# Performance work log

Measured on AMD Instinct MI355X. Metric: run time of the kernel, lower is better.

## Reference

```python
import jax, jax.numpy as jnp
import numpy as np

VOCAB = 100000
TOPK = 20
EMB = 300
BS, SEQ = 64, 256

def setup_inputs() -> dict:
    key = jax.random.key(0)
    k1, k2, k3, k4, k5 = jax.random.split(key, 5)
    conceptnet_text_vec = jax.random.randint(k1, (BS, SEQ), 0, VOCAB)
    neighbors = jax.random.randint(k2, (VOCAB, TOPK), 0, VOCAB)
    emb = jax.random.normal(k3, (VOCAB, EMB), dtype=jnp.float32)
    # xavier-normal init for attention params
    a = jax.random.normal(k4, (EMB, EMB), dtype=jnp.float32) * np.sqrt(2.0 / (EMB + EMB))
    b = jax.random.normal(k5, (EMB, 1), dtype=jnp.float32) * np.sqrt(2.0 / (EMB + 1))
    return {"conceptnet_text_vec": conceptnet_text_vec, "neighbors": neighbors,
            "emb": emb, "a": a, "b": b}

def reference(conceptnet_text_vec, neighbors, emb, a, b):
    # double gather: ids -> neighbor ids -> neighbor embeddings
    nb = neighbors[conceptnet_text_vec]          # [B, S, K] int
    h = emb[nb]                                  # [B, S, K, D]
    # tanh attention scores over the K (neighbor) dim
    e = jnp.einsum('bske,e->bsk', jnp.tanh(jnp.einsum('bskd,de->bske', h, a)), b[:, 0])
    att = jax.nn.softmax(e, axis=-1)             # [B, S, K]
    return jnp.einsum('bsk,bskd->bsd', att, h)   # [B, S, D]
```

## Files before the change

kernel.cpp:

```cpp
#include <hip/hip_runtime.h>
#include <hip/hip_bf16.h>
#include <math.h>

#define VOCAB 100000
#define TOPK  20
#define EMB   300
#define NTOK  (64*256)
#define NB    1563
#define NSLICE 128

typedef __attribute__((ext_vector_type(8))) short short8;
typedef __attribute__((ext_vector_type(4))) short short4v;
typedef __attribute__((ext_vector_type(4))) float f32x4;

static __device__ inline short f2bf(float f) {
    __hip_bfloat16 h = __float2bfloat16(f);
    short s; __builtin_memcpy(&s, &h, 2);
    return s;
}

__global__ void prep_kernel(const float* __restrict__ A, short* __restrict__ aT)
{
    const int e = blockIdx.x;
    for (int d = threadIdx.x; d < 320; d += 256) {
        float f = (e < EMB && d < EMB) ? A[(size_t)d * EMB + e] : 0.f;
        aT[e * 320 + d] = f2bf(f);
    }
}

__global__ __launch_bounds__(512, 1) void score_kernel(
    const float* __restrict__ emb, const short* __restrict__ aT,
    const float* __restrict__ B, float* __restrict__ S0, float* __restrict__ S1)
{
    __shared__ short8 EsS[64 * 40];
    __shared__ float4 Scr[2 * 5 * 4 * 64];
    __shared__ float  Sred[128];

    const int t     = threadIdx.x;
    const int eh    = blockIdx.x >> 7;
    const int slice = blockIdx.x & 127;

    const int lid = t & 63;
    const int w   = t >> 6;
    const int kh  = w >> 2;
    const int mg  = (w >> 1) & 1;
    const int ng  = w & 1;
    const int lm  = lid & 15;
    const int lk  = lid >> 4;
    const int kb    = kh * 20;
    const int xmask = lm & 7;
    const int cell  = mg * 2 + ng;

    const short8* aT8 = (const short8*)aT;
    short8 bAll[5][5];
#pragma unroll
    for (int g = 0; g < 5; ++g) {
        const int e = eh * 160 + ng * 80 + g * 16 + lm;
#pragma unroll
        for (int ks = 0; ks < 5; ++ks)
            bAll[g][ks] = aT8[e * 40 + kb + ks * 4 + lk];
    }

    float bcol[5];
#pragma unroll
    for (int g = 0; g < 5; ++g) {
        const int e = eh * 160 + ng * 80 + g * 16 + lm;
        bcol[g] = (e < EMB) ? B[e] : 0.f;
    }
    int rb[2];
#pragma unroll
    for (int mt = 0; mt < 2; ++mt)
        rb[mt] = (mg * 32 + mt * 16 + lm) * 40;

    const int ntiles = (NB - slice + NSLICE - 1) / NSLICE;

    float4 pf[5][2]; float4 pft;

#define ISSUE_PF(tn) do {                                                     \
    const float4* esrc = (const float4*)(emb + (size_t)(tn) * 64 * EMB);      \
    _Pragma("unroll")                                                         \
    for (int j = 0; j < 5; ++j) {                                             \
        const int i = t + j * 512;                                            \
        const int row = i / 37, cc = i - row * 37;                            \
        const bool ok = (i < 2368) && ((tn) * 64 + row < VOCAB);              \
        pf[j][0] = ok ? esrc[row * 75 + cc * 2]     : make_float4(0,0,0,0);   \
        pf[j][1] = ok ? esrc[row * 75 + cc * 2 + 1] : make_float4(0,0,0,0);   \
    }                                                                         \
    if (t < 64) pft = ((tn) * 64 + t < VOCAB) ? esrc[t * 75 + 74]             \
                                              : make_float4(0,0,0,0);         \
} while (0)

#define STAGE() do {                                                          \
    _Pragma("unroll")                                                         \
    for (int j = 0; j < 5; ++j) {                                             \
        const int i = t + j * 512;                                            \
        if (i < 2368) {                                                       \
            const int row = i / 37, cc = i - row * 37;                        \
            short8 val;                                                       \
            val[0]=f2bf(pf[j][0].x); val[1]=f2bf(pf[j][0].y);                 \
            val[2]=f2bf(pf[j][0].z); val[3]=f2bf(pf[j][0].w);                 \
            val[4]=f2bf(pf[j][1].x); val[5]=f2bf(pf[j][1].y);                 \
            val[6]=f2bf(pf[j][1].z); val[7]=f2bf(pf[j][1].w);                 \
            EsS[row * 40 + (cc ^ (row & 7))] = val;                           \
        }                                                                     \
    }                                                                         \
    if (t < 64) {                                                             \
        short4v h; h.x=f2bf(pft.x); h.y=f2bf(pft.y);                          \
        h.z=f2bf(pft.z); h.w=f2bf(pft.w);                                     \
        short* base = (short*)&EsS[t * 40 + (37 ^ (t & 7))];                  \
        *(short4v*)(base) = h;                                                \
        *(short4v*)(base + 4) = (short4v){0,0,0,0};                           \
    }                                                                         \
    if (t < 128) {                                                            \
        const int row = t >> 1, cc = 38 + (t & 1);                            \
        EsS[row * 40 + (cc ^ (row & 7))] = (short8){0,0,0,0,0,0,0,0};         \
    }                                                                         \
} while (0)

    ISSUE_PF(slice);
    STAGE();
    ISSUE_PF(slice + NSLICE);
    __syncthreads();

    for (int tt = 0; tt < ntiles; ++tt) {
        const int tile = slice + tt * NSLICE;
        const int v0   = tile * 64;

        f32x4 acc0[5], acc1[5];
#pragma unroll
        for (int g = 0; g < 5; ++g) {
            acc0[g] = (f32x4){0.f, 0.f, 0.f, 0.f};
            acc1[g] = (f32x4){0.f, 0.f, 0.f, 0.f};
        }
        short8 afr[2][2];
        {
            const int kx = (kb + lk) ^ xmask;
            afr[0][0] = EsS[rb[0] + kx];
            afr[0][1] = EsS[rb[1] + kx];
        }
#pragma unroll
        for (int ks = 0; ks < 5; ++ks) {
            const int cur = ks & 1, nx = cur ^ 1;
            if (ks < 4) {
                const int kx = (kb + (ks + 1) * 4 + lk) ^ xmask;
                afr[nx][0] = EsS[rb[0] + kx];
                afr[nx][1] = EsS[rb[1] + kx];
            }
#pragma unroll
            for (int g = 0; g < 5; ++g) {
                acc0[g] = __builtin_amdgcn_mfma_f32_16x16x32_bf16(
                              afr[cur][0], bAll[g][ks], acc0[g], 0, 0, 0);
                acc1[g] = __builtin_amdgcn_mfma_f32_16x16x32_bf16(
                              afr[cur][1], bAll[g][ks], acc1[g], 0, 0, 0);
            }
        }
        __syncthreads();

        if (kh == 0) {
#pragma unroll
            for (int g = 0; g < 5; ++g)
                Scr[((0 * 5 + g) * 4 + cell) * 64 + lid] = *(float4*)&acc1[g];
        } else {
#pragma unroll
            for (int g = 0; g < 5; ++g)
                Scr[((1 * 5 + g) * 4 + cell) * 64 + lid] = *(float4*)&acc0[g];
        }
        if (tt + 1 < ntiles) {
            STAGE();
            ISSUE_PF(slice + (tt + 2) * NSLICE);
        }
        __syncthreads();

        float part[4];
        if (kh == 0) {
#pragma unroll
            for (int i = 0; i < 4; ++i) {
                float p = 0.f;
#pragma unroll
                for (int g = 0; g < 5; ++g) {
                    float4 o = Scr[((1 * 5 + g) * 4 + cell) * 64 + lid];
                    float x  = acc0[g][i] + ((const float*)&o)[i];
                    float xc = fminf(fmaxf(x, -15.f), 15.f);
                    float e2 = __expf(2.f * xc);
                    p += __fdividef(e2 - 1.f, e2 + 1.f) * bcol[g];
                }
                part[i] = p;
            }
        } else {
#pragma unroll
            for (int i = 0; i < 4; ++i) {
                float p = 0.f;
#pragma unroll
                for (int g = 0; g < 5; ++g) {
                    float4 o = Scr[((0 * 5 + g) * 4 + cell) * 64 + lid];
                    float x  = acc1[g][i] + ((const float*)&o)[i];
                    float xc = fminf(fmaxf(x, -15.f), 15.f);
                    float e2 = __expf(2.f * xc);
                    p += __fdividef(e2 - 1.f, e2 + 1.f) * bcol[g];
                }
                part[i] = p;
            }
        }
#pragma unroll
        for (int m = 1; m <= 8; m <<= 1)
#pragma unroll
            for (int i = 0; i < 4; ++i)
                part[i] += __shfl_xor(part[i], m);
        if (lm == 0) {
#pragma unroll
            for (int i = 0; i < 4; ++i)
                Sred[ng * 64 + mg * 32 + kh * 16 + lk * 4 + i] = part[i];
        }
        __syncthreads();

        if (t < 64) {
            const int v = v0 + t;
            if (v < VOCAB) {
                float* Sp = eh ? S1 : S0;
                Sp[v] = Sred[t] + Sred[64 + t];
            }
        }
    }
#undef ISSUE_PF
#undef STAGE
}

__global__ __launch_bounds__(256) void attend_kernel(
    const int* __restrict__ text, const int* __restrict__ neighbors,
    const float* __restrict__ emb, const float* __restrict__ S0,
    const float* __restrict__ S1, float* __restrict__ out)
{
    const int lane = threadIdx.x & 63;
    const int wv   = threadIdx.x >> 6;
    const int tok  = blockIdx.x * 4 + wv;

    const int tid = text[tok];

    int   nbk = 0;
    float sc  = -1e30f;
    if (lane < TOPK) {
        nbk = neighbors[tid * TOPK + lane];
        sc  = S0[nbk] + S1[nbk];
    }

    float mx = sc;
#pragma unroll
    for (int m = 16; m >= 1; m >>= 1)
        mx = fmaxf(mx, __shfl_xor(mx, m));

    float ex = (lane < TOPK) ? expf(sc - mx) : 0.f;
    float sum = ex;
#pragma unroll
    for (int m = 16; m >= 1; m >>= 1)
        sum += __shfl_xor(sum, m);
    float att = ex / sum;

    float acc0 = 0.f, acc1 = 0.f, acc2 = 0.f, acc3 = 0.f, acc4 = 0.f;
    const bool has5 = (lane < EMB - 256);
#pragma unroll 4
    for (int k = 0; k < TOPK; ++k) {
        const float wgt = __shfl(att, k);
        const int   id  = __shfl(nbk, k);
        const float* row = emb + (size_t)id * EMB;
        acc0 = fmaf(wgt, row[lane      ], acc0);
        acc1 = fmaf(wgt, row[lane +  64], acc1);
        acc2 = fmaf(wgt, row[lane + 128], acc2);
        acc3 = fmaf(wgt, row[lane + 192], acc3);
        if (has5) acc4 = fmaf(wgt, row[lane + 256], acc4);
    }

    float* orow = out + (size_t)tok * EMB;
    orow[lane      ] = acc0;
    orow[lane +  64] = acc1;
    orow[lane + 128] = acc2;
    orow[lane + 192] = acc3;
    if (has5) orow[lane + 256] = acc4;
}

extern "C" void kernel_launch(void* const* d_in, const int* in_sizes, int n_in,
                              void* d_out, int out_size, void* d_ws, size_t ws_size,
                              hipStream_t stream) {
    const int*   text      = (const int*)d_in[0];
    const int*   neighbors = (const int*)d_in[1];
    const float* emb       = (const float*)d_in[2];
    const float* A         = (const float*)d_in[3];
    const float* B         = (const float*)d_in[4];
    float*       out       = (float*)d_out;

    char* ws = (char*)d_ws;
    float* S0 = (float*)ws;
    float* S1 = (float*)(ws + 400000);
    short* aT = (short*)(ws + 800000);

    prep_kernel<<<320, 256, 0, stream>>>(A, aT);
    score_kernel<<<256, 512, 0, stream>>>(emb, aT, B, S0, S1);
    attend_kernel<<<NTOK / 4, 256, 0, stream>>>(text, neighbors, emb, S0, S1, out);
}
```

Baseline: 142.9 us.

## Restructure score kernel: 1024-thread blocks, B matrix in LDS, more blocks

The score kernel now launches 512 blocks of 1024 threads instead of 256 blocks of 512. Each block stages its half of the transposed A matrix into shared memory, and B fragments are read from LDS per k-step instead of being held in 25 registers per thread. Each wave now covers a single 16-row M tile, and the cross-k-half reduction scratch reuses the embedding tile buffer. The prefetch depth drops from two tiles ahead to one. The aim is to cut register pressure and raise parallelism, at the cost of more LDS traffic, an extra barrier per tile and less latency hiding on the emb loads.

```diff
diff --git a/kernel.cpp b/kernel.cpp
--- a/kernel.cpp
+++ b/kernel.cpp
@@ -7,7 +7,7 @@
 #define EMB   300
 #define NTOK  (64*256)
 #define NB    1563
-#define NSLICE 128
+#define NVG   256
 
 typedef __attribute__((ext_vector_type(8))) short short8;
 typedef __attribute__((ext_vector_type(4))) short short4v;
@@ -28,188 +28,155 @@
     }
 }
 
-__global__ __launch_bounds__(512, 1) void score_kernel(
+__global__ __launch_bounds__(1024, 1) void score_kernel(
     const float* __restrict__ emb, const short* __restrict__ aT,
     const float* __restrict__ B, float* __restrict__ S0, float* __restrict__ S1)
 {
+    __shared__ short8 BsS[160 * 40];
     __shared__ short8 EsS[64 * 40];
-    __shared__ float4 Scr[2 * 5 * 4 * 64];
     __shared__ float  Sred[128];
 
-    const int t     = threadIdx.x;
-    const int eh    = blockIdx.x >> 7;
-    const int slice = blockIdx.x & 127;
+    const int t  = threadIdx.x;
+    const int eh = blockIdx.x & 1;
+    const int vg = blockIdx.x >> 1;
+
+    const short8* aT8 = (const short8*)aT;
+#pragma unroll
+    for (int j = 0; j < 7; ++j) {
+        const int i = t + j * 1024;
+        if (i < 6400) {
+            const int col = i / 40, q = i - col * 40;
+            BsS[col * 40 + (q ^ (col & 7))] = aT8[(eh * 160 + col) * 40 + q];
+        }
+    }
 
     const int lid = t & 63;
     const int w   = t >> 6;
-    const int kh  = w >> 2;
-    const int mg  = (w >> 1) & 1;
+    const int kh  = w >> 3;
+    const int mg  = (w >> 1) & 3;
     const int ng  = w & 1;
     const int lm  = lid & 15;
     const int lk  = lid >> 4;
-    const int kb    = kh * 20;
-    const int xmask = lm & 7;
-    const int cell  = mg * 2 + ng;
-
-    const short8* aT8 = (const short8*)aT;
-    short8 bAll[5][5];
+    const int kb  = kh * 20;
+    const int xm  = lm & 7;
+    const int cell = mg * 2 + ng;
+
+    const int rbA = (mg * 16 + lm) * 40;
+    int rbB[5]; float bcol[5];
 #pragma unroll
     for (int g = 0; g < 5; ++g) {
-        const int e = eh * 160 + ng * 80 + g * 16 + lm;
-#pragma unroll
-        for (int ks = 0; ks < 5; ++ks)
-            bAll[g][ks] = aT8[e * 40 + kb + ks * 4 + lk];
-    }
-
-    float bcol[5];
-#pragma unroll
-    for (int g = 0; g < 5; ++g) {
-        const int e = eh * 160 + ng * 80 + g * 16 + lm;
+        const int col = ng * 80 + g * 16 + lm;
+        rbB[g] = col * 40;
+        const int e = eh * 160 + col;
         bcol[g] = (e < EMB) ? B[e] : 0.f;
     }
-    int rb[2];
-#pragma unroll
-    for (int mt = 0; mt < 2; ++mt)
-        rb[mt] = (mg * 32 + mt * 16 + lm) * 40;
-
-    const int ntiles = (NB - slice + NSLICE - 1) / NSLICE;
-
-    float4 pf[5][2]; float4 pft;
-
-#define ISSUE_PF(tn) do {                                                     \
-    const float4* esrc = (const float4*)(emb + (size_t)(tn) * 64 * EMB);      \
+
+    const int ntiles = (NB - vg + NVG - 1) / NVG;
+
+    float4 pf[3][2]; float4 pft;
+
+#define ISSUE_PF(TT) do {                                                     \
+    const float4* esrc = (const float4*)(emb + (size_t)(TT) * 64 * EMB);      \
     _Pragma("unroll")                                                         \
-    for (int j = 0; j < 5; ++j) {                                             \
-        const int i = t + j * 512;                                            \
-        const int row = i / 37, cc = i - row * 37;                            \
-        const bool ok = (i < 2368) && ((tn) * 64 + row < VOCAB);              \
-        pf[j][0] = ok ? esrc[row * 75 + cc * 2]     : make_float4(0,0,0,0);   \
-        pf[j][1] = ok ? esrc[row * 75 + cc * 2 + 1] : make_float4(0,0,0,0);   \
-    }                                                                         \
-    if (t < 64) pft = ((tn) * 64 + t < VOCAB) ? esrc[t * 75 + 74]             \
+    for (int j = 0; j < 3; ++j) {                                             \
+        const int i = t + j * 1024;                                           \
+        const int row = i / 37, c = i - row * 37;                             \
+        const bool ok = (i < 2368) && ((TT) * 64 + row < VOCAB);              \
+        pf[j][0] = ok ? esrc[row * 75 + c * 2]     : make_float4(0,0,0,0);    \
+        pf[j][1] = ok ? esrc[row * 75 + c * 2 + 1] : make_float4(0,0,0,0);    \
+    }                                                                         \
+    if (t < 64) pft = ((TT) * 64 + t < VOCAB) ? esrc[t * 75 + 74]             \
                                               : make_float4(0,0,0,0);         \
 } while (0)
 
 #define STAGE() do {                                                          \
     _Pragma("unroll")                                                         \
-    for (int j = 0; j < 5; ++j) {                                             \
-        const int i = t + j * 512;                                            \
+    for (int j = 0; j < 3; ++j) {                                             \
+        const int i = t + j * 1024;                                           \
         if (i < 2368) {                                                       \
-            const int row = i / 37, cc = i - row * 37;                        \
+            const int row = i / 37, c = i - row * 37;                         \
             short8 val;                                                       \
             val[0]=f2bf(pf[j][0].x); val[1]=f2bf(pf[j][0].y);                 \
             val[2]=f2bf(pf[j][0].z); val[3]=f2bf(pf[j][0].w);                 \
             val[4]=f2bf(pf[j][1].x); val[5]=f2bf(pf[j][1].y);                 \
             val[6]=f2bf(pf[j][1].z); val[7]=f2bf(pf[j][1].w);                 \
-            EsS[row * 40 + (cc ^ (row & 7))] = val;                           \
+            EsS[row * 40 + (c ^ (row & 7))] = val;                            \
         }                                                                     \
     }                                                                         \
-    if (t < 64) {                                                             \
-        short4v h; h.x=f2bf(pft.x); h.y=f2bf(pft.y);                          \
-        h.z=f2bf(pft.z); h.w=f2bf(pft.w);                                     \
-        short* base = (short*)&EsS[t * 40 + (37 ^ (t & 7))];                  \
-        *(short4v*)(base) = h;                                                \
-        *(short4v*)(base + 4) = (short4v){0,0,0,0};                           \
-    }                                                                         \
-    if (t < 128) {                                                            \
-        const int row = t >> 1, cc = 38 + (t & 1);                            \
-        EsS[row * 40 + (cc ^ (row & 7))] = (short8){0,0,0,0,0,0,0,0};         \
+    if (t < 64) {                   \
+        short8 v37 = (short8){0,0,0,0,0,0,0,0};                               \
+        v37[0]=f2bf(pft.x); v37[1]=f2bf(pft.y);                               \
+        v37[2]=f2bf(pft.z); v37[3]=f2bf(pft.w);                               \
+        EsS[t * 40 + (37 ^ (t & 7))] = v37;                                   \
+    }                                                                         \
+    if (t < 128) {                           \
+        const int row = t >> 1, q = 38 + (t & 1);                             \
+        EsS[row * 40 + (q ^ (row & 7))] = (short8){0,0,0,0,0,0,0,0};          \
     }                                                                         \
 } while (0)
 
-    ISSUE_PF(slice);
+    ISSUE_PF(vg);
     STAGE();
-    ISSUE_PF(slice + NSLICE);
-    __syncthreads();
 
     for (int tt = 0; tt < ntiles; ++tt) {
-        const int tile = slice + tt * NSLICE;
-        const int v0   = tile * 64;
-
-        f32x4 acc0[5], acc1[5];
-#pragma unroll
-        for (int g = 0; g < 5; ++g) {
-            acc0[g] = (f32x4){0.f, 0.f, 0.f, 0.f};
-            acc1[g] = (f32x4){0.f, 0.f, 0.f, 0.f};
-        }
-        short8 afr[2][2];
-        {
-            const int kx = (kb + lk) ^ xmask;
-            afr[0][0] = EsS[rb[0] + kx];
-            afr[0][1] = EsS[rb[1] + kx];
-        }
+        const int v0 = (vg + tt * NVG) * 64;
+
+        __syncthreads();
+        if (tt + 1 < ntiles) ISSUE_PF(vg + (tt + 1) * NVG);
+
+        f32x4 acc[5];
+#pragma unroll
+        for (int g = 0; g < 5; ++g) acc[g] = (f32x4){0.f, 0.f, 0.f, 0.f};
+
+        short8 afr[2];
+        afr[0] = EsS[rbA + ((kb + lk) ^ xm)];
 #pragma unroll
         for (int ks = 0; ks < 5; ++ks) {
             const int cur = ks & 1, nx = cur ^ 1;
-            if (ks < 4) {
-                const int kx = (kb + (ks + 1) * 4 + lk) ^ xmask;
-                afr[nx][0] = EsS[rb[0] + kx];
-                afr[nx][1] = EsS[rb[1] + kx];
-            }
+            if (ks < 4)
+                afr[nx] = EsS[rbA + ((kb + (ks + 1) * 4 + lk) ^ xm)];
+            short8 bfr[5];
+            const int sx = (kb + ks * 4 + lk) ^ xm;
+#pragma unroll
+            for (int g = 0; g < 5; ++g) bfr[g] = BsS[rbB[g] + sx];
+#pragma unroll
+            for (int g = 0; g < 5; ++g)
+                acc[g] = __builtin_amdgcn_mfma_f32_16x16x32_bf16(
+                             afr[cur], bfr[g], acc[g], 0, 0, 0);
+        }
+        __syncthreads();
+
+        float4* ScrF = (float4*)EsS;
+        if (kh == 1) {
+#pragma unroll
+            for (int g = 0; g < 5; ++g)
+                ScrF[(g * 8 + cell) * 64 + lid] = *(float4*)&acc[g];
+        }
+        __syncthreads();
+
+        if (kh == 0) {
+            float part[4] = {0.f, 0.f, 0.f, 0.f};
 #pragma unroll
             for (int g = 0; g < 5; ++g) {
-                acc0[g] = __builtin_amdgcn_mfma_f32_16x16x32_bf16(
-                              afr[cur][0], bAll[g][ks], acc0[g], 0, 0, 0);
-                acc1[g] = __builtin_amdgcn_mfma_f32_16x16x32_bf16(
-                              afr[cur][1], bAll[g][ks], acc1[g], 0, 0, 0);
-            }
-        }
-        __syncthreads();
-
-        if (kh == 0) {
-#pragma unroll
-            for (int g = 0; g < 5; ++g)
-                Scr[((0 * 5 + g) * 4 + cell) * 64 + lid] = *(float4*)&acc1[g];
-        } else {
-#pragma unroll
-            for (int g = 0; g < 5; ++g)
-                Scr[((1 * 5 + g) * 4 + cell) * 64 + lid] = *(float4*)&acc0[g];
-        }
-        if (tt + 1 < ntiles) {
-            STAGE();
-            ISSUE_PF(slice + (tt + 2) * NSLICE);
-        }
-        __syncthreads();
-
-        float part[4];
-        if (kh == 0) {
-#pragma unroll
-            for (int i = 0; i < 4; ++i) {
-                float p = 0.f;
-#pragma unroll
-                for (int g = 0; g < 5; ++g) {
-                    float4 o = Scr[((1 * 5 + g) * 4 + cell) * 64 + lid];
-                    float x  = acc0[g][i] + ((const float*)&o)[i];
+                float4 o = ScrF[(g * 8 + cell) * 64 + lid];
+#pragma unroll
+                for (int i = 0; i < 4; ++i) {
+                    float x  = acc[g][i] + (&o.x)[i];
                     float xc = fminf(fmaxf(x, -15.f), 15.f);
                     float e2 = __expf(2.f * xc);
-                    p += __fdividef(e2 - 1.f, e2 + 1.f) * bcol[g];
+                    part[i] += __fdividef(e2 - 1.f, e2 + 1.f) * bcol[g];
                 }
-                part[i] = p;
             }
-        } else {
-#pragma unroll
-            for (int i = 0; i < 4; ++i) {
-                float p = 0.f;
-#pragma unroll
-                for (int g = 0; g < 5; ++g) {
-                    float4 o = Scr[((0 * 5 + g) * 4 + cell) * 64 + lid];
-                    float x  = acc1[g][i] + ((const float*)&o)[i];
-                    float xc = fminf(fmaxf(x, -15.f), 15.f);
-                    float e2 = __expf(2.f * xc);
-                    p += __fdividef(e2 - 1.f, e2 + 1.f) * bcol[g];
-                }
-                part[i] = p;
+#pragma unroll
+            for (int m = 1; m <= 8; m <<= 1)
+#pragma unroll
+                for (int i = 0; i < 4; ++i)
+                    part[i] += __shfl_xor(part[i], m);
+            if (lm == 0) {
+#pragma unroll
+                for (int i = 0; i < 4; ++i)
+                    Sred[ng * 64 + mg * 16 + lk * 4 + i] = part[i];
             }
-        }
-#pragma unroll
-        for (int m = 1; m <= 8; m <<= 1)
-#pragma unroll
-            for (int i = 0; i < 4; ++i)
-                part[i] += __shfl_xor(part[i], m);
-        if (lm == 0) {
-#pragma unroll
-            for (int i = 0; i < 4; ++i)
-                Sred[ng * 64 + mg * 32 + kh * 16 + lk * 4 + i] = part[i];
         }
         __syncthreads();
 
@@ -220,6 +187,7 @@
                 Sp[v] = Sred[t] + Sred[64 + t];
             }
         }
+        if (tt + 1 < ntiles) STAGE();
     }
 #undef ISSUE_PF
 #undef STAGE
@@ -293,6 +261,6 @@
     short* aT = (short*)(ws + 800000);
 
     prep_kernel<<<320, 256, 0, stream>>>(A, aT);
-    score_kernel<<<256, 512, 0, stream>>>(emb, aT, B, S0, S1);
+    score_kernel<<<2 * NVG, 1024, 0, stream>>>(emb, aT, B, S0, S1);
     attend_kernel<<<NTOK / 4, 256, 0, stream>>>(text, neighbors, emb, S0, S1, out);
 }
```

New measurement: 133.9 us. -6.3%, faster.
